# Kernel tuning notes

Measured on AMD Instinct MI355X. Metric: run time of the kernel, lower is better.

Reference implementation:

```python
import jax, jax.numpy as jnp
import numpy as np
from jax import lax

B, T, D, A, H, C, K = 32, 1500, 512, 512, 4, 10, 100  # batch, frames, key/query/value dim, attn dim, heads, conv channels, conv half-kernel


def setup_inputs() -> dict:
    rng = jax.random.key(0)
    ks = jax.random.split(rng, 13)
    s = 0.02  # param init scale
    return {
        "key": jax.random.normal(ks[0], (B, T, D), jnp.float32),
        "key_lens": jax.random.randint(ks[1], (B,), 3 * T // 4, T + 1, jnp.int32),
        "value": jax.random.normal(ks[2], (B, T, D), jnp.float32),
        "query": jax.random.normal(ks[3], (B, 1, D), jnp.float32),
        "aw": jax.random.uniform(ks[4], (H, B, T), jnp.float32),
        # shared-across-heads linear params (ModuleList([m]*n_heads) shares one module)
        "w_enc_W": jax.random.normal(ks[5], (D, A), jnp.float32) * s,
        "w_enc_b": jnp.zeros((A,), jnp.float32),
        "w_dec_W": jax.random.normal(ks[6], (D, A), jnp.float32) * s,
        "w_conv_W": jax.random.normal(ks[7], (C, A), jnp.float32) * s,
        "v_W": jax.random.normal(ks[8], (A,), jnp.float32) * s,
        # distinct conv kernel per head: grouped-conv layout [H*C, 1, 2K+1]
        "conv_W": jax.random.normal(ks[9], (H * C, 1, 2 * K + 1), jnp.float32) * s,
        "w_out_W": jax.random.normal(ks[10], (D * H, D), jnp.float32) * s,
        "w_out_b": jnp.zeros((D,), jnp.float32),
    }


def reference(key, key_lens, value, query, aw, w_enc_W, w_enc_b, w_dec_W,
              w_conv_W, v_W, conv_W, w_out_W, w_out_b):
    bs, key_len, _ = key.shape
    n_heads = aw.shape[0]
    half_k = (conv_W.shape[-1] - 1) // 2

    # key projection (shared weights => identical key_a for every head): [B,T,A]
    key_a = jnp.einsum('btd,da->bta', key, w_enc_W) + w_enc_b
    # query projection (no bias): [B,1,A]
    dec = jnp.einsum('bqd,da->bqa', query, w_dec_W)

    # location conv feature: distinct kernel per head via grouped 1D conv
    x = jnp.transpose(aw, (1, 0, 2))  # [B,H,T]
    conv_out = lax.conv_general_dilated(
        x, conv_W, window_strides=(1,), padding=[(half_k, half_k)],
        feature_group_count=n_heads,
        dimension_numbers=('NCH', 'OIH', 'NCH'))  # [B,H*C,T]
    conv_feat = jnp.transpose(
        conv_out.reshape(bs, n_heads, -1, key_len), (1, 0, 3, 2))  # [H,B,T,C]
    conv_proj = jnp.einsum('hbtc,ca->hbta', conv_feat, w_conv_W)  # [H,B,T,A]

    # additive score with tanh, reduced by v: [H,B,T]
    e = jnp.einsum('hbta,a->hbt',
                   jnp.tanh(key_a[None] + dec[None] + conv_proj), v_W)

    # length mask + softmax (sharpening_factor=1, no sigmoid smoothing)
    mask = jnp.arange(key_len) < key_lens[:, None]  # [B,T]
    e = jnp.where(mask[None], e, -jnp.inf)
    aw_new = jax.nn.softmax(e, axis=-1)  # [H,B,T]

    # NOTE: source uses the INPUT aw for the context (quirk preserved)
    ctx = jnp.einsum('hbt,btv->bhv', aw, value)  # [B,H,V]
    ctx = ctx.reshape(bs, 1, -1)  # head-major concat, [B,1,H*V]
    out = jnp.einsum('bqk,kd->bqd', ctx, w_out_W) + w_out_b  # [B,1,D]
    return out, aw_new
```

## Files before the change

kernel.cpp:

```cpp
#include <hip/hip_runtime.h>
#include <hip/hip_bf16.h>

#define BB 32
#define TT 1500
#define DD 512
#define AA 512
#define HH 4
#define CC 10
#define KK 100
#define KW 201
#define MM (BB*TT)
#define PS 2.8853900817779268f

typedef unsigned short u16;
typedef unsigned int u32;
typedef __attribute__((ext_vector_type(8))) short bf16x8;
typedef __attribute__((ext_vector_type(4))) float f32x4;
typedef __attribute__((ext_vector_type(4))) unsigned int u32x4;

static __device__ __forceinline__ u16 f2bf(float f) {
    u32 x = __float_as_uint(f);
    return (u16)((x + 0x7fffu + ((x >> 16) & 1u)) >> 16);
}
static __device__ __forceinline__ u32 pkbf(float lo, float hi) {
    u32 r;
    asm("v_cvt_pk_bf16_f32 %0, %1, %2" : "=v"(r) : "v"(lo), "v"(hi));
    return r;
}
static __device__ __forceinline__ void stage16(const void* g, void* l) {
    __builtin_amdgcn_global_load_lds(
        (const __attribute__((address_space(1))) void*)g,
        (__attribute__((address_space(3))) void*)l, 16, 0, 0);
}

__global__ __launch_bounds__(256) void prep_k(
    const float* __restrict__ wencW, const float* __restrict__ q,
    const float* __restrict__ wdec, const float* __restrict__ encb,
    const float* __restrict__ aw, const float* __restrict__ convW,
    u16* __restrict__ wenc_t, float* __restrict__ dec_ps,
    float* __restrict__ cfeat, float* __restrict__ ctx, float* __restrict__ outz)
{
    __shared__ float pls[4160];
    int blk = blockIdx.x, tid = threadIdx.x;
    if (blk < 64) {
        int a0 = (blk & 7) * 64, d0 = (blk >> 3) * 64;
#pragma unroll
        for (int it = 0; it < 16; ++it) {
            int row = it * 4 + (tid >> 6), col = tid & 63;
            pls[row * 65 + col] = wencW[(size_t)(d0 + row) * AA + a0 + col];
        }
        __syncthreads();
#pragma unroll
        for (int it = 0; it < 16; ++it) {
            int ar = it * 4 + (tid >> 6), dc = tid & 63;
            wenc_t[(size_t)(a0 + ar) * DD + d0 + dc] = f2bf(pls[dc * 65 + ar] * PS);
        }
    } else if (blk < 128) {
        int bidx = blk - 64;
        int b = bidx >> 1, a = (bidx & 1) * 256 + tid;
        for (int i = tid; i < DD; i += 256) pls[i] = q[b * DD + i];
        __syncthreads();
        float acc = encb[a];
#pragma unroll 8
        for (int d = 0; d < DD; ++d) acc = fmaf(pls[d], wdec[(size_t)d * AA + a], acc);
        dec_ps[b * AA + a] = acc * PS;
    } else if (blk < 896) {
        int cidx = blk - 128;
        int hb = cidx / 6, chunk = cidx - hb * 6;
        int h = hb >> 5, b = hb & 31;
        float* srow = pls;
        float* swk  = pls + 456;
        int tstart = chunk * 250;
        const float* arow = aw + (size_t)(h * BB + b) * TT;
        for (int i = tid; i < 450; i += 256) {
            int t = tstart + i - KK;
            srow[i] = (t >= 0 && t < TT) ? arow[t] : 0.f;
        }
        for (int i = tid; i < CC * KW; i += 256) swk[i] = convW[h * CC * KW + i];
        __syncthreads();
        if (tid < 250) {
            float acc[CC];
#pragma unroll
            for (int c = 0; c < CC; ++c) acc[c] = 0.f;
            for (int j = 0; j < KW; ++j) {
                float x = srow[tid + j];
#pragma unroll
                for (int c = 0; c < CC; ++c)
                    acc[c] = fmaf(x, swk[c * KW + j], acc[c]);
            }
            float* dst = cfeat + ((size_t)h * MM + (size_t)b * TT + tstart + tid) * CC;
#pragma unroll
            for (int c = 0; c < CC; ++c) dst[c] = acc[c];
        }
    } else if (blk < 904) {
        float4* p = (float4*)ctx;
        int bidx = blk - 896;
        float4 z = {0.f, 0.f, 0.f, 0.f};
#pragma unroll
        for (int k2 = 0; k2 < 8; ++k2) p[bidx * 2048 + k2 * 256 + tid] = z;
    } else {
        float4* p = (float4*)outz;
        int bidx = blk - 904;
        float4 z = {0.f, 0.f, 0.f, 0.f};
#pragma unroll
        for (int k2 = 0; k2 < 8; ++k2) p[bidx * 2048 + k2 * 256 + tid] = z;
    }
}

__global__ __launch_bounds__(256) void gemm_e_k(
    const float* __restrict__ key, const u16* __restrict__ Bt,
    const float* __restrict__ dec_ps, const float* __restrict__ cf,
    const float* __restrict__ wconv, const float* __restrict__ vw,
    float* __restrict__ Q4)
{
    __shared__ u32x4 smem4[1665];
    char* smem = (char*)smem4;

    int tid = threadIdx.x;
    int orig = blockIdx.x;
    int xcd = orig & 7, idx = orig >> 3;
    int swz = xcd * 375 + idx;
    int bn = swz & 3, bm = swz >> 2;
    int row0 = bm * 64, col0 = bn * 128;
    int lane = tid & 63, wv = tid >> 6;
    int wr = wv >> 1, wc = wv & 1;
    int lhi = lane >> 4, llo = lane & 15;

    f32x4 acc[2][4];
#pragma unroll
    for (int i = 0; i < 2; ++i)
#pragma unroll
        for (int j = 0; j < 4; ++j) acc[i][j] = (f32x4){0.f, 0.f, 0.f, 0.f};

    const float4* gA = (const float4*)(key + (size_t)(row0 + (tid >> 2)) * DD) + (tid & 3) * 2;
    u32 aWoff = (tid >> 2) * 80 + (tid & 3) * 16;
    const u16* gBa = Bt + (size_t)(col0 + (tid & 127)) * DD + (tid >> 7) * 8;
    const u16* gBb = gBa + 16;

    auto stageB = [&](int s, int bbyte) {
        stage16(gBa + s * 32, (u16*)(smem + bbyte) + (size_t)tid * 8);
        stage16(gBb + s * 32, (u16*)(smem + bbyte + 4096) + (size_t)tid * 8);
    };
    auto writeA = [&](int abyte, float4 q0, float4 q1) {
        u32x4 s0;
        s0.x = pkbf(q0.x, q0.y); s0.y = pkbf(q0.z, q0.w);
        s0.z = pkbf(q1.x, q1.y); s0.w = pkbf(q1.z, q1.w);
        *(u32x4*)(smem + abyte + aWoff) = s0;
    };
    auto kstep = [&](int aoff, int boff) {
        bf16x8 af[2], bfr[4];
#pragma unroll
        for (int i = 0; i < 2; ++i)
            af[i] = *(const bf16x8*)(smem + aoff + (wr * 32 + i * 16 + llo) * 80 + lhi * 16);
#pragma unroll
        for (int j = 0; j < 4; ++j)
            bfr[j] = *(const bf16x8*)(smem + boff + (wc * 64 + j * 16 + llo) * 16 + lhi * 2048);
#pragma unroll
        for (int i = 0; i < 2; ++i)
#pragma unroll
            for (int j = 0; j < 4; ++j)
                acc[i][j] = __builtin_amdgcn_mfma_f32_16x16x32_bf16(
                    af[i], bfr[j], acc[i][j], 0, 0, 0);
    };

    float4 p0 = gA[0], p1 = gA[1];
    stageB(0, 10240);
    writeA(0, p0, p1);
    p0 = gA[8]; p1 = gA[9];
    __syncthreads();

#pragma unroll
    for (int t = 0; t < 16; ++t) {
        const int abuf_c = (t & 1) ? 5120 : 0;
        const int bbuf_c = (t & 1) ? 18432 : 10240;
        if (t < 15) {
            const int abuf_n = (t & 1) ? 0 : 5120;
            const int bbuf_n = (t & 1) ? 10240 : 18432;
            stageB(t + 1, bbuf_n);
            writeA(abuf_n, p0, p1);
            if (t < 14) { p0 = gA[(t + 2) * 8]; p1 = gA[(t + 2) * 8 + 1]; }
        }
        kstep(abuf_c, bbuf_c);
        __syncthreads();
    }

    const int ZPAD = 26624;
    int b0 = row0 / TT;
    int boundary = (b0 + 1) * TT - row0;
    int b1 = min(b0 + 1, BB - 1);
    {
        int h = tid >> 6, r = tid & 63;
        const float2* cp = (const float2*)(cf + ((size_t)h * MM + row0 + r) * CC);
        float2 c0 = cp[0], c1 = cp[1], c2 = cp[2], c3 = cp[3], c4 = cp[4];
        u32x4 lo, hi;
        lo.x = pkbf(c0.x, c0.y); lo.y = pkbf(c1.x, c1.y);
        lo.z = pkbf(c2.x, c2.y); lo.w = pkbf(c3.x, c3.y);
        hi.x = pkbf(c4.x, c4.y);
        hi.y = (r < boundary) ? 0x00003f80u : 0x3f800000u;
        hi.z = 0u; hi.w = 0u;
        char* dst = smem + (h * 64 + r) * 48;
        *(u32x4*)dst = lo;
        *(u32x4*)(dst + 16) = hi;
        int col = tid >> 1, kh = tid & 1;
        u32x4 w;
        if (kh == 0) {
            float v0 = wconv[0 * AA + col0 + col] * PS, v1 = wconv[1 * AA + col0 + col] * PS;
            float v2 = wconv[2 * AA + col0 + col] * PS, v3 = wconv[3 * AA + col0 + col] * PS;
            float v4 = wconv[4 * AA + col0 + col] * PS, v5 = wconv[5 * AA + col0 + col] * PS;
            float v6 = wconv[6 * AA + col0 + col] * PS, v7 = wconv[7 * AA + col0 + col] * PS;
            w.x = pkbf(v0, v1); w.y = pkbf(v2, v3); w.z = pkbf(v4, v5); w.w = pkbf(v6, v7);
        } else {
            float v8 = wconv[8 * AA + col0 + col] * PS, v9 = wconv[9 * AA + col0 + col] * PS;
            float d0v = dec_ps[b0 * AA + col0 + col], d1v = dec_ps[b1 * AA + col0 + col];
            w.x = pkbf(v8, v9); w.y = pkbf(d0v, d1v); w.z = 0u; w.w = 0u;
        }
        *(u32x4*)(smem + 12288 + col * 48 + kh * 16) = w;
        if (tid == 0) { *(u32x4*)(smem + ZPAD) = (u32x4){0u, 0u, 0u, 0u}; }
    }
    __syncthreads();

    float svj[4];
    bf16x8 be[4];
#pragma unroll
    for (int j = 0; j < 4; ++j) {
        int col = wc * 64 + j * 16 + llo;
        svj[j] = vw[col0 + col];
        u32 off = (lhi < 2) ? (12288u + col * 48 + lhi * 16) : (u32)ZPAD;
        be[j] = *(const bf16x8*)(smem + off);
    }
#pragma unroll
    for (int h = 0; h < 4; ++h) {
#pragma unroll
        for (int i = 0; i < 2; ++i) {
            int rowA = h * 64 + wr * 32 + i * 16 + llo;
            u32 offa = (lhi < 2) ? (rowA * 48 + lhi * 16) : (u32)ZPAD;
            bf16x8 ae = *(const bf16x8*)(smem + offa);
            float ep[4] = {0.f, 0.f, 0.f, 0.f};
#pragma unroll
            for (int j = 0; j < 4; ++j) {
                f32x4 t4 = __builtin_amdgcn_mfma_f32_16x16x32_bf16(ae, be[j], acc[i][j], 0, 0, 0);
#pragma unroll
                for (int r = 0; r < 4; ++r) {
                    float z = exp2f(t4[r]);
                    float p = __builtin_amdgcn_rcpf(1.f + z);
                    ep[r] = fmaf(svj[j], p, ep[r]);
                }
            }
#pragma unroll
            for (int r = 0; r < 4; ++r) {
                float s = ep[r];
                s += __shfl_xor(s, 1);
                s += __shfl_xor(s, 2);
                s += __shfl_xor(s, 4);
                s += __shfl_xor(s, 8);
                if (llo == 0)
                    Q4[((size_t)(bn * HH + h)) * MM + row0 + wr * 32 + i * 16 + lhi * 4 + r] = s;
            }
        }
    }
}

__global__ __launch_bounds__(256) void fin_k(
    const float* __restrict__ Q4, const int* __restrict__ klen,
    const float* __restrict__ aw, const float* __restrict__ value,
    float* __restrict__ aw_new, float* __restrict__ ctx)
{
    __shared__ float fls[1512];
    int blk = blockIdx.x, tid = threadIdx.x;
    if (blk < 128) {
        int h = blk >> 5, b = blk & 31;
        int len = klen[b];
        const float* q0 = Q4 + (size_t)(0 * HH + h) * MM + (size_t)b * TT;
        const float* q1 = Q4 + (size_t)(1 * HH + h) * MM + (size_t)b * TT;
        const float* q2 = Q4 + (size_t)(2 * HH + h) * MM + (size_t)b * TT;
        const float* q3 = Q4 + (size_t)(3 * HH + h) * MM + (size_t)b * TT;
        float* orow = aw_new + (size_t)(h * BB + b) * TT;
        float* rbuf = fls + 1500;
        int lane = tid & 63, wvv = tid >> 6;
        float mx = -3.4e38f;
        for (int t = tid; t < len; t += 256) {
            float e = -2.f * (q0[t] + q1[t] + q2[t] + q3[t]);
            fls[t] = e;
            mx = fmaxf(mx, e);
        }
#pragma unroll
        for (int off = 32; off; off >>= 1) mx = fmaxf(mx, __shfl_xor(mx, off));
        if (lane == 0) rbuf[wvv] = mx;
        __syncthreads();
        mx = fmaxf(fmaxf(rbuf[0], rbuf[1]), fmaxf(rbuf[2], rbuf[3]));
        float sum = 0.f;
        for (int t = tid; t < len; t += 256) {
            float p = __expf(fls[t] - mx);
            fls[t] = p; sum += p;
        }
#pragma unroll
        for (int off = 32; off; off >>= 1) sum += __shfl_xor(sum, off);
        if (lane == 0) rbuf[4 + wvv] = sum;
        __syncthreads();
        float inv = 1.f / (rbuf[4] + rbuf[5] + rbuf[6] + rbuf[7]);
        for (int t = tid; t < TT; t += 256) orow[t] = (t < len) ? fls[t] * inv : 0.f;
    } else {
        int cidx = blk - 128;
        int b = cidx / 25, chunk = cidx - b * 25;
        int c0 = chunk * 60;
        float (*sw)[60] = (float(*)[60])fls;
        if (tid < 240)
            sw[tid / 60][tid % 60] = aw[(size_t)((tid / 60) * BB + b) * TT + c0 + (tid % 60)];
        __syncthreads();
        float a00 = 0, a01 = 0, a10 = 0, a11 = 0, a20 = 0, a21 = 0, a30 = 0, a31 = 0;
        const float* vp = value + ((size_t)b * TT + c0) * DD;
        for (int t = 0; t < 60; ++t) {
            float v0 = vp[(size_t)t * DD + tid];
            float v1 = vp[(size_t)t * DD + tid + 256];
            a00 = fmaf(sw[0][t], v0, a00); a01 = fmaf(sw[0][t], v1, a01);
            a10 = fmaf(sw[1][t], v0, a10); a11 = fmaf(sw[1][t], v1, a11);
            a20 = fmaf(sw[2][t], v0, a20); a21 = fmaf(sw[2][t], v1, a21);
            a30 = fmaf(sw[3][t], v0, a30); a31 = fmaf(sw[3][t], v1, a31);
        }
        atomicAdd(&ctx[(b * HH + 0) * DD + tid], a00);
        atomicAdd(&ctx[(b * HH + 0) * DD + tid + 256], a01);
        atomicAdd(&ctx[(b * HH + 1) * DD + tid], a10);
        atomicAdd(&ctx[(b * HH + 1) * DD + tid + 256], a11);
        atomicAdd(&ctx[(b * HH + 2) * DD + tid], a20);
        atomicAdd(&ctx[(b * HH + 2) * DD + tid + 256], a21);
        atomicAdd(&ctx[(b * HH + 3) * DD + tid], a30);
        atomicAdd(&ctx[(b * HH + 3) * DD + tid + 256], a31);
    }
}

__global__ __launch_bounds__(512) void out_k(const float* __restrict__ ctx,
                                             const float* __restrict__ wout,
                                             const float* __restrict__ wob,
                                             float* __restrict__ out)
{
    int b0 = blockIdx.x * 4, kc = blockIdx.y;
    int tid = threadIdx.x;
    __shared__ float sc[4][64];
    if (tid < 256) sc[tid >> 6][tid & 63] =
        ctx[(size_t)(b0 + (tid >> 6)) * (HH * DD) + kc * 64 + (tid & 63)];
    __syncthreads();
    float acc0 = 0, acc1 = 0, acc2 = 0, acc3 = 0;
    const float* wp = wout + (size_t)(kc * 64) * DD + tid;
#pragma unroll 8
    for (int kk = 0; kk < 64; ++kk) {
        float w = wp[(size_t)kk * DD];
        acc0 = fmaf(sc[0][kk], w, acc0); acc1 = fmaf(sc[1][kk], w, acc1);
        acc2 = fmaf(sc[2][kk], w, acc2); acc3 = fmaf(sc[3][kk], w, acc3);
    }
    if (kc == 0) {
        float bb = wob[tid];
        acc0 += bb; acc1 += bb; acc2 += bb; acc3 += bb;
    }
    atomicAdd(&out[(b0 + 0) * DD + tid], acc0);
    atomicAdd(&out[(b0 + 1) * DD + tid], acc1);
    atomicAdd(&out[(b0 + 2) * DD + tid], acc2);
    atomicAdd(&out[(b0 + 3) * DD + tid], acc3);
}

extern "C" void kernel_launch(void* const* d_in, const int* in_sizes, int n_in,
                              void* d_out, int out_size, void* d_ws, size_t ws_size,
                              hipStream_t stream) {
    const float* key    = (const float*)d_in[0];
    const int*   klen   = (const int*)  d_in[1];
    const float* value  = (const float*)d_in[2];
    const float* query  = (const float*)d_in[3];
    const float* aw     = (const float*)d_in[4];
    const float* wencW  = (const float*)d_in[5];
    const float* wencb  = (const float*)d_in[6];
    const float* wdecW  = (const float*)d_in[7];
    const float* wconvW = (const float*)d_in[8];
    const float* vW     = (const float*)d_in[9];
    const float* convW  = (const float*)d_in[10];
    const float* woutW  = (const float*)d_in[11];
    const float* woutb  = (const float*)d_in[12];

    float* out    = (float*)d_out;
    float* aw_new = out + BB * DD;

    char* ws = (char*)d_ws;
    u16*   wenc_t = (u16*)ws;
    float* dec_ps = (float*)(ws + 524288);
    float* cfeat  = (float*)(ws + 589824);
    float* Q4     = (float*)(ws + 8269824);
    float* ctx    = (float*)(ws + 11341824);

    prep_k  <<<906, 256, 0, stream>>>(wencW, query, wdecW, wencb, aw, convW,
                                      wenc_t, dec_ps, cfeat, ctx, out);
    gemm_e_k<<<3000, 256, 0, stream>>>(key, wenc_t, dec_ps, cfeat, wconvW, vW, Q4);
    fin_k   <<<928, 256, 0, stream>>>(Q4, klen, aw, value, aw_new, ctx);
    out_k   <<<dim3(8, 32), 512, 0, stream>>>(ctx, woutW, woutb, out);
}
```

Baseline: 360.5 us.

## Pre-convert key to bf16 and triple-buffer GEMM loads via direct-to-LDS

Adds a pass in the prep kernel that converts the whole fp32 key tensor to bf16 in workspace. The GEMM then stages both A and B operands with global_load_lds into a three-stage ring with an XOR-swizzled A layout, and waits with vmcnt/barrier instead of register loads plus conversion and a syncthreads per step. The aim is to remove register pressure and conversion work from the main loop and deepen prefetch. The cost is an extra full write and re-read of a roughly 49 MB bf16 copy of key, plus more LDS per block.

Measured after the change: 371.9 us. 3.2% more time.

```diff
diff --git a/kernel.cpp b/kernel.cpp
--- a/kernel.cpp
+++ b/kernel.cpp
@@ -34,16 +34,27 @@
 }
 
 __global__ __launch_bounds__(256) void prep_k(
-    const float* __restrict__ wencW, const float* __restrict__ q,
-    const float* __restrict__ wdec, const float* __restrict__ encb,
-    const float* __restrict__ aw, const float* __restrict__ convW,
-    u16* __restrict__ wenc_t, float* __restrict__ dec_ps,
-    float* __restrict__ cfeat, float* __restrict__ ctx, float* __restrict__ outz)
+    const float* __restrict__ key, const float* __restrict__ wencW,
+    const float* __restrict__ q, const float* __restrict__ wdec,
+    const float* __restrict__ encb, const float* __restrict__ aw,
+    const float* __restrict__ convW,
+    u16* __restrict__ keybf, u16* __restrict__ wenc_t,
+    float* __restrict__ dec_ps, float* __restrict__ cfeat,
+    float* __restrict__ ctx, float* __restrict__ outz)
 {
     __shared__ float pls[4160];
     int blk = blockIdx.x, tid = threadIdx.x;
-    if (blk < 64) {
-        int a0 = (blk & 7) * 64, d0 = (blk >> 3) * 64;
+    if (blk < 12000) {
+        size_t i = (size_t)blk * 2048 + (size_t)tid * 8;
+        const float4* p = (const float4*)key + i / 4;
+        float4 x = p[0], y = p[1];
+        u32x4 o;
+        o.x = pkbf(x.x, x.y); o.y = pkbf(x.z, x.w);
+        o.z = pkbf(y.x, y.y); o.w = pkbf(y.z, y.w);
+        *(u32x4*)(keybf + i) = o;
+    } else if (blk < 12064) {
+        int t2 = blk - 12000;
+        int a0 = (t2 & 7) * 64, d0 = (t2 >> 3) * 64;
 #pragma unroll
         for (int it = 0; it < 16; ++it) {
             int row = it * 4 + (tid >> 6), col = tid & 63;
@@ -55,8 +66,8 @@
             int ar = it * 4 + (tid >> 6), dc = tid & 63;
             wenc_t[(size_t)(a0 + ar) * DD + d0 + dc] = f2bf(pls[dc * 65 + ar] * PS);
         }
-    } else if (blk < 128) {
-        int bidx = blk - 64;
+    } else if (blk < 12128) {
+        int bidx = blk - 12064;
         int b = bidx >> 1, a = (bidx & 1) * 256 + tid;
         for (int i = tid; i < DD; i += 256) pls[i] = q[b * DD + i];
         __syncthreads();
@@ -64,8 +75,8 @@
 #pragma unroll 8
         for (int d = 0; d < DD; ++d) acc = fmaf(pls[d], wdec[(size_t)d * AA + a], acc);
         dec_ps[b * AA + a] = acc * PS;
-    } else if (blk < 896) {
-        int cidx = blk - 128;
+    } else if (blk < 12896) {
+        int cidx = blk - 12128;
         int hb = cidx / 6, chunk = cidx - hb * 6;
         int h = hb >> 5, b = hb & 31;
         float* srow = pls;
@@ -92,15 +103,15 @@
 #pragma unroll
             for (int c = 0; c < CC; ++c) dst[c] = acc[c];
         }
-    } else if (blk < 904) {
+    } else if (blk < 12904) {
         float4* p = (float4*)ctx;
-        int bidx = blk - 896;
+        int bidx = blk - 12896;
         float4 z = {0.f, 0.f, 0.f, 0.f};
 #pragma unroll
         for (int k2 = 0; k2 < 8; ++k2) p[bidx * 2048 + k2 * 256 + tid] = z;
     } else {
         float4* p = (float4*)outz;
-        int bidx = blk - 904;
+        int bidx = blk - 12904;
         float4 z = {0.f, 0.f, 0.f, 0.f};
 #pragma unroll
         for (int k2 = 0; k2 < 8; ++k2) p[bidx * 2048 + k2 * 256 + tid] = z;
@@ -108,12 +119,12 @@
 }
 
 __global__ __launch_bounds__(256) void gemm_e_k(
-    const float* __restrict__ key, const u16* __restrict__ Bt,
+    const u16* __restrict__ Abf, const u16* __restrict__ Bt,
     const float* __restrict__ dec_ps, const float* __restrict__ cf,
     const float* __restrict__ wconv, const float* __restrict__ vw,
     float* __restrict__ Q4)
 {
-    __shared__ u32x4 smem4[1665];
+    __shared__ u32x4 smem4[2306];
     char* smem = (char*)smem4;
 
     int tid = threadIdx.x;
@@ -132,29 +143,32 @@
 #pragma unroll
         for (int j = 0; j < 4; ++j) acc[i][j] = (f32x4){0.f, 0.f, 0.f, 0.f};
 
-    const float4* gA = (const float4*)(key + (size_t)(row0 + (tid >> 2)) * DD) + (tid & 3) * 2;
-    u32 aWoff = (tid >> 2) * 80 + (tid & 3) * 16;
-    const u16* gBa = Bt + (size_t)(col0 + (tid & 127)) * DD + (tid >> 7) * 8;
-    const u16* gBb = gBa + 16;
-
-    auto stageB = [&](int s, int bbyte) {
-        stage16(gBa + s * 32, (u16*)(smem + bbyte) + (size_t)tid * 8);
-        stage16(gBb + s * 32, (u16*)(smem + bbyte + 4096) + (size_t)tid * 8);
+    int srow = tid >> 2, sslot = tid & 3;
+    int sks = sslot ^ ((srow >> 1) & 3);
+    const u16* aSrc = Abf + (size_t)(row0 + srow) * DD + sks * 8;
+    int bcol = tid & 127, bkc = tid >> 7;
+    const u16* bSrc0 = Bt + (size_t)(col0 + bcol) * DD + bkc * 8;
+    const u16* bSrc1 = bSrc0 + 16;
+
+    int arow0 = wr * 32 + llo, arow1 = arow0 + 16;
+    u32 aOff0 = arow0 * 64 + ((lhi ^ ((arow0 >> 1) & 3)) << 4);
+    u32 aOff1 = arow1 * 64 + ((lhi ^ ((arow1 >> 1) & 3)) << 4);
+    u32 bOffB = 4096u + lhi * 2048 + (wc * 64 + llo) * 16;
+
+    auto stage = [&](int g) {
+        char* gb = smem + (g % 3) * 12288;
+        stage16(aSrc + g * 32, gb + tid * 16);
+        stage16(bSrc0 + g * 32, gb + 4096 + tid * 16);
+        stage16(bSrc1 + g * 32, gb + 8192 + tid * 16);
     };
-    auto writeA = [&](int abyte, float4 q0, float4 q1) {
-        u32x4 s0;
-        s0.x = pkbf(q0.x, q0.y); s0.y = pkbf(q0.z, q0.w);
-        s0.z = pkbf(q1.x, q1.y); s0.w = pkbf(q1.z, q1.w);
-        *(u32x4*)(smem + abyte + aWoff) = s0;
-    };
-    auto kstep = [&](int aoff, int boff) {
+    auto kstep = [&](int g) {
+        char* gb = smem + (g % 3) * 12288;
         bf16x8 af[2], bfr[4];
-#pragma unroll
-        for (int i = 0; i < 2; ++i)
-            af[i] = *(const bf16x8*)(smem + aoff + (wr * 32 + i * 16 + llo) * 80 + lhi * 16);
+        af[0] = *(const bf16x8*)(gb + aOff0);
+        af[1] = *(const bf16x8*)(gb + aOff1);
 #pragma unroll
         for (int j = 0; j < 4; ++j)
-            bfr[j] = *(const bf16x8*)(smem + boff + (wc * 64 + j * 16 + llo) * 16 + lhi * 2048);
+            bfr[j] = *(const bf16x8*)(gb + bOffB + j * 256);
 #pragma unroll
         for (int i = 0; i < 2; ++i)
 #pragma unroll
@@ -163,28 +177,18 @@
                     af[i], bfr[j], acc[i][j], 0, 0, 0);
     };
 
-    float4 p0 = gA[0], p1 = gA[1];
-    stageB(0, 10240);
-    writeA(0, p0, p1);
-    p0 = gA[8]; p1 = gA[9];
+    stage(0);
+    stage(1);
+#pragma unroll
+    for (int t = 0; t < 16; ++t) {
+        if (t < 15) asm volatile("s_waitcnt vmcnt(3)\ns_barrier" ::: "memory");
+        else        asm volatile("s_waitcnt vmcnt(0)\ns_barrier" ::: "memory");
+        if (t < 14) stage(t + 2);
+        kstep(t);
+    }
+
     __syncthreads();
-
-#pragma unroll
-    for (int t = 0; t < 16; ++t) {
-        const int abuf_c = (t & 1) ? 5120 : 0;
-        const int bbuf_c = (t & 1) ? 18432 : 10240;
-        if (t < 15) {
-            const int abuf_n = (t & 1) ? 0 : 5120;
-            const int bbuf_n = (t & 1) ? 10240 : 18432;
-            stageB(t + 1, bbuf_n);
-            writeA(abuf_n, p0, p1);
-            if (t < 14) { p0 = gA[(t + 2) * 8]; p1 = gA[(t + 2) * 8 + 1]; }
-        }
-        kstep(abuf_c, bbuf_c);
-        __syncthreads();
-    }
-
-    const int ZPAD = 26624;
+    const u32 ZPAD = 36864;
     int b0 = row0 / TT;
     int boundary = (b0 + 1) * TT - row0;
     int b1 = min(b0 + 1, BB - 1);
@@ -225,7 +229,7 @@
     for (int j = 0; j < 4; ++j) {
         int col = wc * 64 + j * 16 + llo;
         svj[j] = vw[col0 + col];
-        u32 off = (lhi < 2) ? (12288u + col * 48 + lhi * 16) : (u32)ZPAD;
+        u32 off = (lhi < 2) ? (12288u + col * 48 + lhi * 16) : ZPAD;
         be[j] = *(const bf16x8*)(smem + off);
     }
 #pragma unroll
@@ -233,7 +237,7 @@
 #pragma unroll
         for (int i = 0; i < 2; ++i) {
             int rowA = h * 64 + wr * 32 + i * 16 + llo;
-            u32 offa = (lhi < 2) ? (rowA * 48 + lhi * 16) : (u32)ZPAD;
+            u32 offa = (lhi < 2) ? (rowA * 48 + lhi * 16) : ZPAD;
             bf16x8 ae = *(const bf16x8*)(smem + offa);
             float ep[4] = {0.f, 0.f, 0.f, 0.f};
 #pragma unroll
@@ -378,15 +382,16 @@
     float* aw_new = out + BB * DD;
 
     char* ws = (char*)d_ws;
-    u16*   wenc_t = (u16*)ws;
-    float* dec_ps = (float*)(ws + 524288);
-    float* cfeat  = (float*)(ws + 589824);
-    float* Q4     = (float*)(ws + 8269824);
-    float* ctx    = (float*)(ws + 11341824);
-
-    prep_k  <<<906, 256, 0, stream>>>(wencW, query, wdecW, wencb, aw, convW,
-                                      wenc_t, dec_ps, cfeat, ctx, out);
-    gemm_e_k<<<3000, 256, 0, stream>>>(key, wenc_t, dec_ps, cfeat, wconvW, vW, Q4);
+    u16*   keybf  = (u16*)ws;
+    u16*   wenc_t = (u16*)(ws + 49152000);
+    float* dec_ps = (float*)(ws + 49676288);
+    float* cfeat  = (float*)(ws + 49741824);
+    float* Q4     = (float*)(ws + 57421824);
+    float* ctx    = (float*)(ws + 60493824);
+
+    prep_k  <<<12912, 256, 0, stream>>>(key, wencW, query, wdecW, wencb, aw, convW,
+                                        keybf, wenc_t, dec_ps, cfeat, ctx, out);
+    gemm_e_k<<<3000, 256, 0, stream>>>(keybf, wenc_t, dec_ps, cfeat, wconvW, vW, Q4);
     fin_k   <<<928, 256, 0, stream>>>(Q4, klen, aw, value, aw_new, ctx);
     out_k   <<<dim3(8, 32), 512, 0, stream>>>(ctx, woutW, woutb, out);
 }
```

## Stage fp32 key tiles directly to LDS with triple-buffered async pipeline

Applied to the files above, without the earlier changes.

The GEMM main loop now copies raw fp32 key tiles into LDS with the async stage16 path instead of loading them into registers and converting to bf16 before the LDS write. The bf16 conversion moves to the point where fragments are read from LDS. A three-stage ring buffer with explicit vmcnt waits and barriers keeps two stages in flight. This removes register staging and the per-step conversion from the load path and deepens prefetch, at the cost of roughly twice the LDS (about 49 KB) and conversion work inside each k-step.

After: 392.7 us. +8.9%, slower.

```diff
diff --git a/kernel.cpp b/kernel.cpp
--- a/kernel.cpp
+++ b/kernel.cpp
@@ -113,7 +113,7 @@
     const float* __restrict__ wconv, const float* __restrict__ vw,
     float* __restrict__ Q4)
 {
-    __shared__ u32x4 smem4[1665];
+    __shared__ u32x4 smem4[3073];
     char* smem = (char*)smem4;
 
     int tid = threadIdx.x;
@@ -132,29 +132,39 @@
 #pragma unroll
         for (int j = 0; j < 4; ++j) acc[i][j] = (f32x4){0.f, 0.f, 0.f, 0.f};
 
-    const float4* gA = (const float4*)(key + (size_t)(row0 + (tid >> 2)) * DD) + (tid & 3) * 2;
-    u32 aWoff = (tid >> 2) * 80 + (tid & 3) * 16;
-    const u16* gBa = Bt + (size_t)(col0 + (tid & 127)) * DD + (tid >> 7) * 8;
-    const u16* gBb = gBa + 16;
-
-    auto stageB = [&](int s, int bbyte) {
-        stage16(gBa + s * 32, (u16*)(smem + bbyte) + (size_t)tid * 8);
-        stage16(gBb + s * 32, (u16*)(smem + bbyte + 4096) + (size_t)tid * 8);
+    const float* aSrc = key + (size_t)(row0 + (tid & 63)) * DD + (tid >> 6) * 4;
+    int bcol = tid & 127, bkc = tid >> 7;
+    const u16* bSrc0 = Bt + (size_t)(col0 + bcol) * DD + bkc * 8;
+    const u16* bSrc1 = bSrc0 + 16;
+
+    u32 aRow0 = (u32)(wr * 32 + llo) * 16 + lhi * 2048;
+    u32 aRow1 = aRow0 + 16 * 16;
+    u32 bOffB = 8192u + lhi * 2048 + (wc * 64 + llo) * 16;
+
+    auto stage = [&](int g) {
+        char* gb = smem + (g % 3) * 16384;
+        stage16(aSrc + g * 32,      gb + tid * 16);
+        stage16(aSrc + g * 32 + 16, gb + 4096 + tid * 16);
+        stage16(bSrc0 + g * 32, gb + 8192 + tid * 16);
+        stage16(bSrc1 + g * 32, gb + 12288 + tid * 16);
     };
-    auto writeA = [&](int abyte, float4 q0, float4 q1) {
-        u32x4 s0;
-        s0.x = pkbf(q0.x, q0.y); s0.y = pkbf(q0.z, q0.w);
-        s0.z = pkbf(q1.x, q1.y); s0.w = pkbf(q1.z, q1.w);
-        *(u32x4*)(smem + abyte + aWoff) = s0;
-    };
-    auto kstep = [&](int aoff, int boff) {
+    auto kstep = [&](int g) {
+        char* gb = smem + (g % 3) * 16384;
+        f32x4 a0l = *(const f32x4*)(gb + aRow0);
+        f32x4 a0h = *(const f32x4*)(gb + aRow0 + 1024);
+        f32x4 a1l = *(const f32x4*)(gb + aRow1);
+        f32x4 a1h = *(const f32x4*)(gb + aRow1 + 1024);
         bf16x8 af[2], bfr[4];
-#pragma unroll
-        for (int i = 0; i < 2; ++i)
-            af[i] = *(const bf16x8*)(smem + aoff + (wr * 32 + i * 16 + llo) * 80 + lhi * 16);
+        u32x4 p0, p1;
+        p0.x = pkbf(a0l[0], a0l[1]); p0.y = pkbf(a0l[2], a0l[3]);
+        p0.z = pkbf(a0h[0], a0h[1]); p0.w = pkbf(a0h[2], a0h[3]);
+        p1.x = pkbf(a1l[0], a1l[1]); p1.y = pkbf(a1l[2], a1l[3]);
+        p1.z = pkbf(a1h[0], a1h[1]); p1.w = pkbf(a1h[2], a1h[3]);
+        af[0] = __builtin_bit_cast(bf16x8, p0);
+        af[1] = __builtin_bit_cast(bf16x8, p1);
 #pragma unroll
         for (int j = 0; j < 4; ++j)
-            bfr[j] = *(const bf16x8*)(smem + boff + (wc * 64 + j * 16 + llo) * 16 + lhi * 2048);
+            bfr[j] = *(const bf16x8*)(gb + bOffB + j * 256);
 #pragma unroll
         for (int i = 0; i < 2; ++i)
 #pragma unroll
@@ -163,28 +173,18 @@
                     af[i], bfr[j], acc[i][j], 0, 0, 0);
     };
 
-    float4 p0 = gA[0], p1 = gA[1];
-    stageB(0, 10240);
-    writeA(0, p0, p1);
-    p0 = gA[8]; p1 = gA[9];
+    stage(0);
+    stage(1);
+#pragma unroll
+    for (int t = 0; t < 16; ++t) {
+        if (t < 15) asm volatile("s_waitcnt vmcnt(4)\ns_barrier" ::: "memory");
+        else        asm volatile("s_waitcnt vmcnt(0)\ns_barrier" ::: "memory");
+        if (t < 14) stage(t + 2);
+        kstep(t);
+    }
+
     __syncthreads();
-
-#pragma unroll
-    for (int t = 0; t < 16; ++t) {
-        const int abuf_c = (t & 1) ? 5120 : 0;
-        const int bbuf_c = (t & 1) ? 18432 : 10240;
-        if (t < 15) {
-            const int abuf_n = (t & 1) ? 0 : 5120;
-            const int bbuf_n = (t & 1) ? 10240 : 18432;
-            stageB(t + 1, bbuf_n);
-            writeA(abuf_n, p0, p1);
-            if (t < 14) { p0 = gA[(t + 2) * 8]; p1 = gA[(t + 2) * 8 + 1]; }
-        }
-        kstep(abuf_c, bbuf_c);
-        __syncthreads();
-    }
-
-    const int ZPAD = 26624;
+    const u32 ZPAD = 49152;
     int b0 = row0 / TT;
     int boundary = (b0 + 1) * TT - row0;
     int b1 = min(b0 + 1, BB - 1);
@@ -225,7 +225,7 @@
     for (int j = 0; j < 4; ++j) {
         int col = wc * 64 + j * 16 + llo;
         svj[j] = vw[col0 + col];
-        u32 off = (lhi < 2) ? (12288u + col * 48 + lhi * 16) : (u32)ZPAD;
+        u32 off = (lhi < 2) ? (12288u + col * 48 + lhi * 16) : ZPAD;
         be[j] = *(const bf16x8*)(smem + off);
     }
 #pragma unroll
@@ -233,7 +233,7 @@
 #pragma unroll
         for (int i = 0; i < 2; ++i) {
             int rowA = h * 64 + wr * 32 + i * 16 + llo;
-            u32 offa = (lhi < 2) ? (rowA * 48 + lhi * 16) : (u32)ZPAD;
+            u32 offa = (lhi < 2) ? (rowA * 48 + lhi * 16) : ZPAD;
             bf16x8 ae = *(const bf16x8*)(smem + offa);
             float ep[4] = {0.f, 0.f, 0.f, 0.f};
 #pragma unroll
```
